# Optimization experiments

Hardware: AMD Instinct MI355X
Metric: run time of the kernel (lower is better)

The kernel has to match this reference:

```python
import jax, jax.numpy as jnp
import numpy as np

N, E, F_IN, F_OUT = 8192, 1024, 256, 256


def setup_inputs() -> dict:
    key = jax.random.key(0)
    k1, k2, k3, k4 = jax.random.split(key, 4)
    X = jax.random.normal(k1, (N, F_IN), dtype=jnp.float32)
    # binary incidence matrix: node i belongs to hyperedge j with p=0.05
    H = (jax.random.uniform(k2, (N, E)) < 0.05).astype(jnp.float32)
    W = jax.random.normal(k3, (F_OUT, F_IN), dtype=jnp.float32) * (1.0 / np.sqrt(F_IN))
    b = jax.random.normal(k4, (F_OUT,), dtype=jnp.float32) * 0.01
    return {"X": X, "H": H, "W": W, "b": b}


def reference(X, H, W, b):
    # Dv = diag(row sums of H), De = diag(col sums of H)
    dv = jnp.sum(H, axis=1)                      # [N] node degrees
    de = jnp.sum(H, axis=0)                      # [E] edge degrees
    dv_inv_sqrt = 1.0 / jnp.sqrt(dv)             # inv of sqrt(Dv) (diagonal)
    de_inv = 1.0 / de                            # inv of De (diagonal)
    # diagonal matrices realized as broadcast scalings (same math, no N x N).
    Xs = X * dv_inv_sqrt[:, None]
    M = H.T @ Xs                                 # H^T (...)          [E, F]
    M = M * de_inv[:, None]                      # De^-1 (...)        [E, F]
    X_new = (H @ M) * dv_inv_sqrt[:, None]       # Dv^-1/2 H (...)    [N, F]
    return X_new @ W.T + b                       # nn.Linear
```

## Files before the change

kernel.cpp:

```cpp
#include <hip/hip_runtime.h>
#include <hip/hip_bf16.h>
#include <stdint.h>

typedef __attribute__((ext_vector_type(8))) short bf16x8;
typedef __attribute__((ext_vector_type(4))) float f32x4;
typedef __attribute__((ext_vector_type(4))) unsigned int u32x4;
typedef __attribute__((ext_vector_type(2))) unsigned int u32x2;
typedef unsigned short u16;
typedef unsigned int u32;
typedef unsigned long long u64;

#define N_NODES 8192
#define N_EDGES 1024
#define F_DIM   256
#define EMAX 512
#define NMAX 128
#define NSEG 512
#define SEGR 16

__device__ __forceinline__ u16 f2bf(float f) {
    union { float f; u32 u; } v; v.f = f;
    u32 u = v.u;
    u = (u + 0x7FFFu + ((u >> 16) & 1u)) >> 16;
    return (u16)u;
}
__device__ __forceinline__ float bflo(u32 p) {
    union { u32 u; float f; } v; v.u = p << 16; return v.f;
}
__device__ __forceinline__ float bfhi(u32 p) {
    union { u32 u; float f; } v; v.u = p & 0xffff0000u; return v.f;
}

__global__ void prep_count(const float* __restrict__ H, const float* __restrict__ X,
                           float* __restrict__ dv, u16* __restrict__ nlist,
                           u16* __restrict__ Xs, u16* __restrict__ cnt_seg) {
    __shared__ u32 colp[4][64][4];
    const int tid = threadIdx.x;
    const int wv = tid >> 6;
    const int lane = tid & 63;
    const int n0 = blockIdx.x * SEGR + wv * 4;

    f32x4 hv[4][4];
    f32x4 xv[4];
#pragma unroll
    for (int r = 0; r < 4; ++r) {
        const int n = n0 + r;
#pragma unroll
        for (int q = 0; q < 4; ++q)
            hv[r][q] = *(const f32x4*)(&H[(size_t)n * N_EDGES + q * 256 + lane * 4]);
        xv[r] = *(const f32x4*)(&X[(size_t)n * F_DIM + lane * 4]);
    }

    u32 cpk[4] = {0u, 0u, 0u, 0u};
#pragma unroll
    for (int r = 0; r < 4; ++r) {
        const int n = n0 + r;
        u32 m16 = 0u;
#pragma unroll
        for (int q = 0; q < 4; ++q)
#pragma unroll
            for (int j = 0; j < 4; ++j) {
                const u32 nz = (hv[r][q][j] != 0.f) ? 1u : 0u;
                m16 |= nz << (q * 4 + j);
                cpk[q] += nz << (8 * j);
            }
        const u32 cl = (u32)__popc(m16);
        u32 x = cl;
#pragma unroll
        for (int d = 1; d < 64; d <<= 1) {
            const u32 t = __shfl_up(x, d, 64);
            if (lane >= d) x += t;
        }
        const u32 total = __shfl(x, 63, 64);
        u32 pos = x - cl;
        u16* nrow = &nlist[(size_t)n * NMAX];
        u32 m = m16;
        while (m) {
            const int bidx = __builtin_ctz(m);
            m &= m - 1;
            const int col = ((bidx >> 2) << 8) + lane * 4 + (bidx & 3);
            if (pos < NMAX) nrow[pos] = (u16)col;
            ++pos;
        }
        if (lane == 0) dv[n] = (float)total;
        const float s = rsqrtf((float)total);
        u32x2 pk;
        pk[0] = (u32)f2bf(xv[r][0] * s) | ((u32)f2bf(xv[r][1] * s) << 16);
        pk[1] = (u32)f2bf(xv[r][2] * s) | ((u32)f2bf(xv[r][3] * s) << 16);
        *(u32x2*)(&Xs[(size_t)n * F_DIM + lane * 4]) = pk;
    }
#pragma unroll
    for (int q = 0; q < 4; ++q) colp[wv][lane][q] = cpk[q];
    __syncthreads();
    const int q = tid >> 6, l = tid & 63;
    const u32 sum = colp[0][l][q] + colp[1][l][q] + colp[2][l][q] + colp[3][l][q];
    const int s = blockIdx.x;
#pragma unroll
    for (int j = 0; j < 4; ++j) {
        const int col = q * 256 + l * 4 + j;
        cnt_seg[(size_t)col * NSEG + s] = (u16)((sum >> (8 * j)) & 0xffu);
    }
}

__global__ void prefix_seg(const u16* __restrict__ cnt_seg, u16* __restrict__ base,
                           u32* __restrict__ cnt_e) {
    const int tid = threadIdx.x;
    const int wv = tid >> 6, lane = tid & 63;
    const int e = blockIdx.x * 4 + wv;
    union { u32x4 v; u16 c[8]; } in;
    in.v = *(const u32x4*)(&cnt_seg[(size_t)e * NSEG + lane * 8]);
    u32 run = 0, pre[8];
#pragma unroll
    for (int k = 0; k < 8; ++k) { pre[k] = run; run += in.c[k]; }
    u32 x = run;
#pragma unroll
    for (int d = 1; d < 64; d <<= 1) {
        const u32 t = __shfl_up(x, d, 64);
        if (lane >= d) x += t;
    }
    const u32 excl = x - run;
    union { u32x4 v; u16 o[8]; } out;
#pragma unroll
    for (int k = 0; k < 8; ++k) out.o[k] = (u16)(excl + pre[k]);
    *(u32x4*)(&base[(size_t)e * NSEG + lane * 8]) = out.v;
    if (lane == 63) cnt_e[e] = x;
}

__global__ void scatter_build(const float* __restrict__ H, const u16* __restrict__ base,
                              u16* __restrict__ elist) {
    const int t = threadIdx.x;
    const int s = blockIdx.x;
    const int c0 = t * 4;
    const int r0 = s * SEGR;
    f32x4 v[16];
#pragma unroll
    for (int rr = 0; rr < SEGR; ++rr)
        v[rr] = *(const f32x4*)(&H[(size_t)(r0 + rr) * N_EDGES + c0]);
    u32 b[4];
#pragma unroll
    for (int j = 0; j < 4; ++j) b[j] = base[(size_t)(c0 + j) * NSEG + s];
#pragma unroll
    for (int rr = 0; rr < SEGR; ++rr) {
        const int r = r0 + rr;
#pragma unroll
        for (int j = 0; j < 4; ++j)
            if (v[rr][j] != 0.f) {
                if (b[j] < EMAX) elist[(size_t)(c0 + j) * EMAX + b[j]] = (u16)r;
                b[j]++;
            }
    }
}

__global__ void spmm1(const u16* __restrict__ Xs, const u32* __restrict__ cnt_e,
                      const u16* __restrict__ elist, float* __restrict__ M) {
    __shared__ u16 lst[EMAX];
    __shared__ float red[16 * F_DIM];
    const int tid = threadIdx.x;
    const int wv = tid >> 6, lane = tid & 63;
    const int e = blockIdx.x;
    const int cnt = min((int)cnt_e[e], EMAX);
    if (tid < 256)
        ((u32*)lst)[tid] = ((const u32*)&elist[(size_t)e * EMAX])[tid];
    __syncthreads();

    const int half = lane >> 5;
    const int l32 = lane & 31;
    const int npairs = (cnt + 1) >> 1;
    const int len = (npairs + 7) >> 3;
    const int p0 = wv * len;
    const int p1 = min(p0 + len, npairs);
    float a[8] = {};
#pragma unroll 4
    for (int p = p0; p < p1; ++p) {
        const int idx = 2 * p + half;
        if (idx < cnt) {
            const int nn = lst[idx];
            const u32x4 pk = *(const u32x4*)(&Xs[(size_t)nn * F_DIM + l32 * 8]);
#pragma unroll
            for (int k = 0; k < 4; ++k) { a[2 * k] += bflo(pk[k]); a[2 * k + 1] += bfhi(pk[k]); }
        }
    }
    f32x4 r0 = {a[0], a[1], a[2], a[3]};
    f32x4 r1 = {a[4], a[5], a[6], a[7]};
    *(f32x4*)(&red[(wv * 2 + half) * F_DIM + l32 * 8]) = r0;
    *(f32x4*)(&red[(wv * 2 + half) * F_DIM + l32 * 8 + 4]) = r1;
    __syncthreads();
    if (tid < F_DIM) {
        float s = 0.f;
#pragma unroll
        for (int w = 0; w < 16; ++w) s += red[w * F_DIM + tid];
        M[(size_t)e * F_DIM + tid] = s;
    }
}

__global__ void gemm_we(const float* __restrict__ M, const u32* __restrict__ cnt_e,
                        const float* __restrict__ W, u16* __restrict__ M2) {
    __shared__ u16 As[64 * 72];
    __shared__ u16 Bs[64 * 72];
    const int tid = threadIdx.x;
    const int lane = tid & 63;
    const int wave = tid >> 6;
    const int wm = wave >> 1, wn = wave & 1;
    const int row16 = lane & 15;
    const int quad = lane >> 4;

    const int e0 = blockIdx.y * 64;
    const int j0 = blockIdx.x * 64;

    const int sr = tid >> 2;
    const int fb = (tid & 3) * 16;

    const float dei = 1.f / (float)cnt_e[e0 + sr];

    f32x4 acc[2][2] = {};

    for (int k = 0; k < 256; k += 64) {
#pragma unroll
        for (int s2 = 0; s2 < 4; ++s2) {
            f32x4 a = *(const f32x4*)(&M[(size_t)(e0 + sr) * F_DIM + k + fb + s2 * 4]);
            u32x2 pk;
            pk[0] = (u32)f2bf(a[0] * dei) | ((u32)f2bf(a[1] * dei) << 16);
            pk[1] = (u32)f2bf(a[2] * dei) | ((u32)f2bf(a[3] * dei) << 16);
            *(u32x2*)(&As[sr * 72 + fb + s2 * 4]) = pk;
            f32x4 w = *(const f32x4*)(&W[(size_t)(j0 + sr) * F_DIM + k + fb + s2 * 4]);
            pk[0] = (u32)f2bf(w[0]) | ((u32)f2bf(w[1]) << 16);
            pk[1] = (u32)f2bf(w[2]) | ((u32)f2bf(w[3]) << 16);
            *(u32x2*)(&Bs[sr * 72 + fb + s2 * 4]) = pk;
        }
        __syncthreads();
#pragma unroll
        for (int ks = 0; ks < 2; ++ks) {
            bf16x8 af[2], bfr[2];
#pragma unroll
            for (int t = 0; t < 2; ++t) {
                af[t]  = *(const bf16x8*)(&As[(wm * 32 + t * 16 + row16) * 72 + ks * 32 + quad * 8]);
                bfr[t] = *(const bf16x8*)(&Bs[(wn * 32 + t * 16 + row16) * 72 + ks * 32 + quad * 8]);
            }
#pragma unroll
            for (int tm = 0; tm < 2; tm++)
#pragma unroll
                for (int tn = 0; tn < 2; tn++)
                    acc[tm][tn] = __builtin_amdgcn_mfma_f32_16x16x32_bf16(
                        af[tm], bfr[tn], acc[tm][tn], 0, 0, 0);
        }
        __syncthreads();
    }

#pragma unroll
    for (int tm = 0; tm < 2; tm++) {
#pragma unroll
        for (int tn = 0; tn < 2; tn++) {
            const int col = j0 + wn * 32 + tn * 16 + row16;
#pragma unroll
            for (int r = 0; r < 4; r++) {
                const int row = e0 + wm * 32 + tm * 16 + quad * 4 + r;
                M2[(size_t)row * F_DIM + col] = f2bf(acc[tm][tn][r]);
            }
        }
    }
}

__global__ void spmm2(const u16* __restrict__ M2, const float* __restrict__ dv,
                      const u16* __restrict__ nlist, const float* __restrict__ bias,
                      float* __restrict__ out) {
    __shared__ u16 nl[4 * NMAX];
    __shared__ float red2[4][2][F_DIM];
    const int tid = threadIdx.x;
    const int wv = tid >> 6, lane = tid & 63;
    const int n = blockIdx.x * 4 + wv;
    if (tid < 256)
        ((u32*)nl)[tid] = ((const u32*)&nlist[(size_t)blockIdx.x * 4 * NMAX])[tid];
    __syncthreads();
    const float dvn = dv[n];
    const int cnt = min((int)dvn, NMAX);
    const u16* lst = &nl[wv * NMAX];
    const int half = lane >> 5;
    const int l32 = lane & 31;
    float a[8] = {};
    const int npairs = (cnt + 1) >> 1;
#pragma unroll 4
    for (int p = 0; p < npairs; ++p) {
        const int idx = 2 * p + half;
        if (idx < cnt) {
            const int e = lst[idx];
            const u32x4 pk = *(const u32x4*)(&M2[(size_t)e * F_DIM + l32 * 8]);
#pragma unroll
            for (int k = 0; k < 4; ++k) { a[2 * k] += bflo(pk[k]); a[2 * k + 1] += bfhi(pk[k]); }
        }
    }
    f32x4 r0 = {a[0], a[1], a[2], a[3]};
    f32x4 r1 = {a[4], a[5], a[6], a[7]};
    *(f32x4*)(&red2[wv][half][l32 * 8]) = r0;
    *(f32x4*)(&red2[wv][half][l32 * 8 + 4]) = r1;
    const float s = rsqrtf(dvn);
    const f32x4 bb = *(const f32x4*)(&bias[lane * 4]);
    f32x4 r;
#pragma unroll
    for (int k = 0; k < 4; ++k)
        r[k] = (red2[wv][0][lane * 4 + k] + red2[wv][1][lane * 4 + k]) * s + bb[k];
    *(f32x4*)(&out[(size_t)n * F_DIM + lane * 4]) = r;
}

extern "C" void kernel_launch(void* const* d_in, const int* in_sizes, int n_in,
                              void* d_out, int out_size, void* d_ws, size_t ws_size,
                              hipStream_t stream) {
    (void)in_sizes; (void)n_in; (void)out_size; (void)ws_size;
    const float* X = (const float*)d_in[0];
    const float* H = (const float*)d_in[1];
    const float* W = (const float*)d_in[2];
    const float* b = (const float*)d_in[3];
    float* out = (float*)d_out;

    char* ws = (char*)d_ws;
    float* dv      = (float*)(ws);
    u32*   cnt_e   = (u32*)(ws + 0x8000);
    u16*   cnt_seg = (u16*)(ws + 0x10000);
    u16*   base    = (u16*)(ws + 0x110000);
    u16*   nlist   = (u16*)(ws + 0x210000);
    u16*   elist   = (u16*)(ws + 0x410000);
    u16*   Xs      = (u16*)(ws + 0x510000);
    float* M       = (float*)(ws + 0x910000);
    u16*   M2      = (u16*)(ws + 0xA10000);

    prep_count<<<NSEG, 256, 0, stream>>>(H, X, dv, nlist, Xs, cnt_seg);
    prefix_seg<<<256, 256, 0, stream>>>(cnt_seg, base, cnt_e);
    scatter_build<<<NSEG, 256, 0, stream>>>(H, base, elist);
    spmm1<<<N_EDGES, 512, 0, stream>>>(Xs, cnt_e, elist, M);
    gemm_we<<<dim3(4, 16), 256, 0, stream>>>(M, cnt_e, W, M2);
    spmm2<<<N_NODES / 4, 256, 0, stream>>>(M2, dv, nlist, b, out);
}
```

Before: 140.4 us.

## Fuse all six stages into one cooperative persistent kernel with grid syncs

Replaces the six separate kernel launches with a single cooperative kernel of 256 blocks that runs each stage in turn, separated by grid.sync. The second pass over H in scatter_build is removed by caching per-row bitmasks in shared memory. The segment layout changes to 32 rows per block and the prefix scan is reorganised. The aim is to remove launch gaps and the redundant H reread. The cost is that the prefix and GEMM stages now use only 16 or 64 blocks while the rest of the grid waits, and every grid barrier adds overhead.

```diff
diff --git a/kernel.cpp b/kernel.cpp
--- a/kernel.cpp
+++ b/kernel.cpp
@@ -1,6 +1,9 @@
 #include <hip/hip_runtime.h>
+#include <hip/hip_cooperative_groups.h>
 #include <hip/hip_bf16.h>
 #include <stdint.h>
+
+namespace cg = cooperative_groups;
 
 typedef __attribute__((ext_vector_type(8))) short bf16x8;
 typedef __attribute__((ext_vector_type(4))) float f32x4;
@@ -15,8 +18,10 @@
 #define F_DIM   256
 #define EMAX 512
 #define NMAX 128
-#define NSEG 512
-#define SEGR 16
+#define NSEG 256
+#define SEGR 32
+#define NBLK 256
+#define NTHR 512
 
 __device__ __forceinline__ u16 f2bf(float f) {
     union { float f; u32 u; } v; v.f = f;
@@ -31,274 +36,286 @@
     union { u32 u; float f; } v; v.u = p & 0xffff0000u; return v.f;
 }
 
-__global__ void prep_count(const float* __restrict__ H, const float* __restrict__ X,
-                           float* __restrict__ dv, u16* __restrict__ nlist,
-                           u16* __restrict__ Xs, u16* __restrict__ cnt_seg) {
-    __shared__ u32 colp[4][64][4];
+struct SMem {
+    u16 hmask[SEGR][64];
+    union {
+        u32 colp[8][64][4];
+        u32 sums[64][8];
+        struct {
+            u32   lst[4][256];
+            float red[4][4][256];
+        } p4;
+        struct {
+            u16 As[64 * 72];
+            u16 Bs[64 * 72];
+        } p5;
+        struct {
+            u32   nl[2048];
+            float red2[8][2][256];
+        } p6;
+    } u;
+};
+
+__global__ void __launch_bounds__(NTHR) mega(
+    const float* __restrict__ H, const float* __restrict__ X,
+    const float* __restrict__ W, const float* __restrict__ bias,
+    float* __restrict__ out,
+    float* __restrict__ dv, u32* __restrict__ cnt_e,
+    u16* __restrict__ cnt_seg, u16* __restrict__ base,
+    u16* __restrict__ nlist, u16* __restrict__ elist,
+    u16* __restrict__ Xs, float* __restrict__ M, u16* __restrict__ M2)
+{
+    __shared__ SMem sm;
+    cg::grid_group grid = cg::this_grid();
     const int tid = threadIdx.x;
+    const int blk = blockIdx.x;
     const int wv = tid >> 6;
     const int lane = tid & 63;
-    const int n0 = blockIdx.x * SEGR + wv * 4;
-
-    f32x4 hv[4][4];
-    f32x4 xv[4];
-#pragma unroll
-    for (int r = 0; r < 4; ++r) {
-        const int n = n0 + r;
-#pragma unroll
-        for (int q = 0; q < 4; ++q)
-            hv[r][q] = *(const f32x4*)(&H[(size_t)n * N_EDGES + q * 256 + lane * 4]);
-        xv[r] = *(const f32x4*)(&X[(size_t)n * F_DIM + lane * 4]);
-    }
-
-    u32 cpk[4] = {0u, 0u, 0u, 0u};
-#pragma unroll
-    for (int r = 0; r < 4; ++r) {
-        const int n = n0 + r;
-        u32 m16 = 0u;
-#pragma unroll
-        for (int q = 0; q < 4; ++q)
-#pragma unroll
-            for (int j = 0; j < 4; ++j) {
-                const u32 nz = (hv[r][q][j] != 0.f) ? 1u : 0u;
-                m16 |= nz << (q * 4 + j);
-                cpk[q] += nz << (8 * j);
-            }
-        const u32 cl = (u32)__popc(m16);
-        u32 x = cl;
-#pragma unroll
-        for (int d = 1; d < 64; d <<= 1) {
-            const u32 t = __shfl_up(x, d, 64);
-            if (lane >= d) x += t;
-        }
-        const u32 total = __shfl(x, 63, 64);
-        u32 pos = x - cl;
-        u16* nrow = &nlist[(size_t)n * NMAX];
-        u32 m = m16;
-        while (m) {
-            const int bidx = __builtin_ctz(m);
-            m &= m - 1;
-            const int col = ((bidx >> 2) << 8) + lane * 4 + (bidx & 3);
-            if (pos < NMAX) nrow[pos] = (u16)col;
-            ++pos;
-        }
-        if (lane == 0) dv[n] = (float)total;
-        const float s = rsqrtf((float)total);
-        u32x2 pk;
-        pk[0] = (u32)f2bf(xv[r][0] * s) | ((u32)f2bf(xv[r][1] * s) << 16);
-        pk[1] = (u32)f2bf(xv[r][2] * s) | ((u32)f2bf(xv[r][3] * s) << 16);
-        *(u32x2*)(&Xs[(size_t)n * F_DIM + lane * 4]) = pk;
-    }
-#pragma unroll
-    for (int q = 0; q < 4; ++q) colp[wv][lane][q] = cpk[q];
-    __syncthreads();
-    const int q = tid >> 6, l = tid & 63;
-    const u32 sum = colp[0][l][q] + colp[1][l][q] + colp[2][l][q] + colp[3][l][q];
-    const int s = blockIdx.x;
-#pragma unroll
-    for (int j = 0; j < 4; ++j) {
-        const int col = q * 256 + l * 4 + j;
-        cnt_seg[(size_t)col * NSEG + s] = (u16)((sum >> (8 * j)) & 0xffu);
-    }
-}
-
-__global__ void prefix_seg(const u16* __restrict__ cnt_seg, u16* __restrict__ base,
-                           u32* __restrict__ cnt_e) {
-    const int tid = threadIdx.x;
-    const int wv = tid >> 6, lane = tid & 63;
-    const int e = blockIdx.x * 4 + wv;
-    union { u32x4 v; u16 c[8]; } in;
-    in.v = *(const u32x4*)(&cnt_seg[(size_t)e * NSEG + lane * 8]);
-    u32 run = 0, pre[8];
-#pragma unroll
-    for (int k = 0; k < 8; ++k) { pre[k] = run; run += in.c[k]; }
-    u32 x = run;
-#pragma unroll
-    for (int d = 1; d < 64; d <<= 1) {
-        const u32 t = __shfl_up(x, d, 64);
-        if (lane >= d) x += t;
-    }
-    const u32 excl = x - run;
-    union { u32x4 v; u16 o[8]; } out;
-#pragma unroll
-    for (int k = 0; k < 8; ++k) out.o[k] = (u16)(excl + pre[k]);
-    *(u32x4*)(&base[(size_t)e * NSEG + lane * 8]) = out.v;
-    if (lane == 63) cnt_e[e] = x;
-}
-
-__global__ void scatter_build(const float* __restrict__ H, const u16* __restrict__ base,
-                              u16* __restrict__ elist) {
-    const int t = threadIdx.x;
-    const int s = blockIdx.x;
-    const int c0 = t * 4;
-    const int r0 = s * SEGR;
-    f32x4 v[16];
-#pragma unroll
-    for (int rr = 0; rr < SEGR; ++rr)
-        v[rr] = *(const f32x4*)(&H[(size_t)(r0 + rr) * N_EDGES + c0]);
-    u32 b[4];
-#pragma unroll
-    for (int j = 0; j < 4; ++j) b[j] = base[(size_t)(c0 + j) * NSEG + s];
-#pragma unroll
-    for (int rr = 0; rr < SEGR; ++rr) {
-        const int r = r0 + rr;
-#pragma unroll
-        for (int j = 0; j < 4; ++j)
-            if (v[rr][j] != 0.f) {
-                if (b[j] < EMAX) elist[(size_t)(c0 + j) * EMAX + b[j]] = (u16)r;
-                b[j]++;
-            }
-    }
-}
-
-__global__ void spmm1(const u16* __restrict__ Xs, const u32* __restrict__ cnt_e,
-                      const u16* __restrict__ elist, float* __restrict__ M) {
-    __shared__ u16 lst[EMAX];
-    __shared__ float red[16 * F_DIM];
-    const int tid = threadIdx.x;
-    const int wv = tid >> 6, lane = tid & 63;
-    const int e = blockIdx.x;
-    const int cnt = min((int)cnt_e[e], EMAX);
-    if (tid < 256)
-        ((u32*)lst)[tid] = ((const u32*)&elist[(size_t)e * EMAX])[tid];
-    __syncthreads();
-
-    const int half = lane >> 5;
-    const int l32 = lane & 31;
-    const int npairs = (cnt + 1) >> 1;
-    const int len = (npairs + 7) >> 3;
-    const int p0 = wv * len;
-    const int p1 = min(p0 + len, npairs);
-    float a[8] = {};
-#pragma unroll 4
-    for (int p = p0; p < p1; ++p) {
-        const int idx = 2 * p + half;
-        if (idx < cnt) {
-            const int nn = lst[idx];
-            const u32x4 pk = *(const u32x4*)(&Xs[(size_t)nn * F_DIM + l32 * 8]);
-#pragma unroll
-            for (int k = 0; k < 4; ++k) { a[2 * k] += bflo(pk[k]); a[2 * k + 1] += bfhi(pk[k]); }
-        }
-    }
-    f32x4 r0 = {a[0], a[1], a[2], a[3]};
-    f32x4 r1 = {a[4], a[5], a[6], a[7]};
-    *(f32x4*)(&red[(wv * 2 + half) * F_DIM + l32 * 8]) = r0;
-    *(f32x4*)(&red[(wv * 2 + half) * F_DIM + l32 * 8 + 4]) = r1;
-    __syncthreads();
-    if (tid < F_DIM) {
-        float s = 0.f;
-#pragma unroll
-        for (int w = 0; w < 16; ++w) s += red[w * F_DIM + tid];
-        M[(size_t)e * F_DIM + tid] = s;
-    }
-}
-
-__global__ void gemm_we(const float* __restrict__ M, const u32* __restrict__ cnt_e,
-                        const float* __restrict__ W, u16* __restrict__ M2) {
-    __shared__ u16 As[64 * 72];
-    __shared__ u16 Bs[64 * 72];
-    const int tid = threadIdx.x;
-    const int lane = tid & 63;
-    const int wave = tid >> 6;
-    const int wm = wave >> 1, wn = wave & 1;
-    const int row16 = lane & 15;
-    const int quad = lane >> 4;
-
-    const int e0 = blockIdx.y * 64;
-    const int j0 = blockIdx.x * 64;
-
-    const int sr = tid >> 2;
-    const int fb = (tid & 3) * 16;
-
-    const float dei = 1.f / (float)cnt_e[e0 + sr];
-
-    f32x4 acc[2][2] = {};
-
-    for (int k = 0; k < 256; k += 64) {
-#pragma unroll
-        for (int s2 = 0; s2 < 4; ++s2) {
-            f32x4 a = *(const f32x4*)(&M[(size_t)(e0 + sr) * F_DIM + k + fb + s2 * 4]);
+
+    {
+        const int n0 = blk * SEGR + wv * 4;
+        f32x4 hv[4][4], xv[4];
+#pragma unroll
+        for (int r = 0; r < 4; ++r) {
+            const int n = n0 + r;
+#pragma unroll
+            for (int q = 0; q < 4; ++q)
+                hv[r][q] = *(const f32x4*)(&H[(size_t)n * N_EDGES + q * 256 + lane * 4]);
+            xv[r] = *(const f32x4*)(&X[(size_t)n * F_DIM + lane * 4]);
+        }
+        u32 cpk[4] = {0u, 0u, 0u, 0u};
+#pragma unroll
+        for (int r = 0; r < 4; ++r) {
+            const int n = n0 + r;
+            u32 m16 = 0u;
+#pragma unroll
+            for (int q = 0; q < 4; ++q)
+#pragma unroll
+                for (int j = 0; j < 4; ++j) {
+                    const u32 nz = (hv[r][q][j] != 0.f) ? 1u : 0u;
+                    m16 |= nz << (q * 4 + j);
+                    cpk[q] += nz << (8 * j);
+                }
+            sm.hmask[wv * 4 + r][lane] = (u16)m16;
+            const u32 cl = (u32)__popc(m16);
+            u32 x = cl;
+#pragma unroll
+            for (int d = 1; d < 64; d <<= 1) {
+                const u32 t = __shfl_up(x, d, 64);
+                if (lane >= d) x += t;
+            }
+            const u32 total = __shfl(x, 63, 64);
+            u32 pos = x - cl;
+            u16* nrow = &nlist[(size_t)n * NMAX];
+            u32 m = m16;
+            while (m) {
+                const int bidx = __builtin_ctz(m);
+                m &= m - 1;
+                const int col = ((bidx >> 2) << 8) + lane * 4 + (bidx & 3);
+                if (pos < NMAX) nrow[pos] = (u16)col;
+                ++pos;
+            }
+            if (lane == 0) dv[n] = (float)total;
+            const float s = rsqrtf((float)total);
             u32x2 pk;
-            pk[0] = (u32)f2bf(a[0] * dei) | ((u32)f2bf(a[1] * dei) << 16);
-            pk[1] = (u32)f2bf(a[2] * dei) | ((u32)f2bf(a[3] * dei) << 16);
-            *(u32x2*)(&As[sr * 72 + fb + s2 * 4]) = pk;
-            f32x4 w = *(const f32x4*)(&W[(size_t)(j0 + sr) * F_DIM + k + fb + s2 * 4]);
-            pk[0] = (u32)f2bf(w[0]) | ((u32)f2bf(w[1]) << 16);
-            pk[1] = (u32)f2bf(w[2]) | ((u32)f2bf(w[3]) << 16);
-            *(u32x2*)(&Bs[sr * 72 + fb + s2 * 4]) = pk;
-        }
-        __syncthreads();
-#pragma unroll
-        for (int ks = 0; ks < 2; ++ks) {
-            bf16x8 af[2], bfr[2];
-#pragma unroll
-            for (int t = 0; t < 2; ++t) {
-                af[t]  = *(const bf16x8*)(&As[(wm * 32 + t * 16 + row16) * 72 + ks * 32 + quad * 8]);
-                bfr[t] = *(const bf16x8*)(&Bs[(wn * 32 + t * 16 + row16) * 72 + ks * 32 + quad * 8]);
-            }
-#pragma unroll
-            for (int tm = 0; tm < 2; tm++)
-#pragma unroll
-                for (int tn = 0; tn < 2; tn++)
-                    acc[tm][tn] = __builtin_amdgcn_mfma_f32_16x16x32_bf16(
-                        af[tm], bfr[tn], acc[tm][tn], 0, 0, 0);
-        }
-        __syncthreads();
-    }
-
-#pragma unroll
-    for (int tm = 0; tm < 2; tm++) {
-#pragma unroll
-        for (int tn = 0; tn < 2; tn++) {
-            const int col = j0 + wn * 32 + tn * 16 + row16;
-#pragma unroll
-            for (int r = 0; r < 4; r++) {
-                const int row = e0 + wm * 32 + tm * 16 + quad * 4 + r;
-                M2[(size_t)row * F_DIM + col] = f2bf(acc[tm][tn][r]);
-            }
-        }
-    }
-}
-
-__global__ void spmm2(const u16* __restrict__ M2, const float* __restrict__ dv,
-                      const u16* __restrict__ nlist, const float* __restrict__ bias,
-                      float* __restrict__ out) {
-    __shared__ u16 nl[4 * NMAX];
-    __shared__ float red2[4][2][F_DIM];
-    const int tid = threadIdx.x;
-    const int wv = tid >> 6, lane = tid & 63;
-    const int n = blockIdx.x * 4 + wv;
-    if (tid < 256)
-        ((u32*)nl)[tid] = ((const u32*)&nlist[(size_t)blockIdx.x * 4 * NMAX])[tid];
-    __syncthreads();
-    const float dvn = dv[n];
-    const int cnt = min((int)dvn, NMAX);
-    const u16* lst = &nl[wv * NMAX];
-    const int half = lane >> 5;
-    const int l32 = lane & 31;
-    float a[8] = {};
-    const int npairs = (cnt + 1) >> 1;
-#pragma unroll 4
-    for (int p = 0; p < npairs; ++p) {
-        const int idx = 2 * p + half;
-        if (idx < cnt) {
-            const int e = lst[idx];
-            const u32x4 pk = *(const u32x4*)(&M2[(size_t)e * F_DIM + l32 * 8]);
-#pragma unroll
-            for (int k = 0; k < 4; ++k) { a[2 * k] += bflo(pk[k]); a[2 * k + 1] += bfhi(pk[k]); }
-        }
-    }
-    f32x4 r0 = {a[0], a[1], a[2], a[3]};
-    f32x4 r1 = {a[4], a[5], a[6], a[7]};
-    *(f32x4*)(&red2[wv][half][l32 * 8]) = r0;
-    *(f32x4*)(&red2[wv][half][l32 * 8 + 4]) = r1;
-    const float s = rsqrtf(dvn);
-    const f32x4 bb = *(const f32x4*)(&bias[lane * 4]);
-    f32x4 r;
-#pragma unroll
-    for (int k = 0; k < 4; ++k)
-        r[k] = (red2[wv][0][lane * 4 + k] + red2[wv][1][lane * 4 + k]) * s + bb[k];
-    *(f32x4*)(&out[(size_t)n * F_DIM + lane * 4]) = r;
+            pk[0] = (u32)f2bf(xv[r][0] * s) | ((u32)f2bf(xv[r][1] * s) << 16);
+            pk[1] = (u32)f2bf(xv[r][2] * s) | ((u32)f2bf(xv[r][3] * s) << 16);
+            *(u32x2*)(&Xs[(size_t)n * F_DIM + lane * 4]) = pk;
+        }
+#pragma unroll
+        for (int q = 0; q < 4; ++q) sm.u.colp[wv][lane][q] = cpk[q];
+        __syncthreads();
+        if (tid < 256) {
+            const int q = tid >> 6, l = tid & 63;
+            u32 sum = 0;
+#pragma unroll
+            for (int w = 0; w < 8; ++w) sum += sm.u.colp[w][l][q];
+            u32x2 st;
+            st[0] = (sum & 0xffu) | (((sum >> 8) & 0xffu) << 16);
+            st[1] = ((sum >> 16) & 0xffu) | (((sum >> 24) & 0xffu) << 16);
+            *(u32x2*)(&cnt_seg[(size_t)blk * N_EDGES + q * 256 + l * 4]) = st;
+        }
+    }
+    __threadfence();
+    grid.sync();
+
+    if (blk < 16) {
+        const int el = tid & 63;
+        const int ch = tid >> 6;
+        const int e = blk * 64 + el;
+        u32 s1 = 0;
+#pragma unroll 8
+        for (int k = 0; k < 32; ++k)
+            s1 += cnt_seg[(size_t)(ch * 32 + k) * N_EDGES + e];
+        sm.u.sums[el][ch] = s1;
+        __syncthreads();
+        u32 run = 0;
+        for (int cc = 0; cc < ch; ++cc) run += sm.u.sums[el][cc];
+#pragma unroll 8
+        for (int k = 0; k < 32; ++k) {
+            const size_t idx = (size_t)(ch * 32 + k) * N_EDGES + e;
+            const u32 cv = cnt_seg[idx];
+            base[idx] = (u16)run;
+            run += cv;
+        }
+        if (ch == 7) cnt_e[e] = run;
+    }
+    __threadfence();
+    grid.sync();
+
+    {
+        const int c0 = tid * 2;
+        const u32 bb = *(const u32*)(&base[(size_t)blk * N_EDGES + c0]);
+        u32 b0 = bb & 0xffffu, b1 = bb >> 16;
+        const int q = c0 >> 8;
+        const int widx = (c0 & 255) >> 2;
+        const int bit0 = q * 4 + (c0 & 3);
+        const int r0g = blk * SEGR;
+        u16* el0 = &elist[(size_t)c0 * EMAX];
+        u16* el1 = &elist[(size_t)(c0 + 1) * EMAX];
+#pragma unroll 8
+        for (int r = 0; r < SEGR; ++r) {
+            const u32 mrow = sm.hmask[r][widx];
+            if ((mrow >> bit0) & 1u) { if (b0 < EMAX) el0[b0] = (u16)(r0g + r); b0++; }
+            if ((mrow >> (bit0 + 1)) & 1u) { if (b1 < EMAX) el1[b1] = (u16)(r0g + r); b1++; }
+        }
+    }
+    __threadfence();
+    grid.sync();
+
+    {
+        const int g = wv >> 1;
+        const int w2 = wv & 1;
+        const int e = blk * 4 + g;
+        const int tg = w2 * 64 + lane;
+        sm.u.p4.lst[g][tg]       = ((const u32*)&elist[(size_t)e * EMAX])[tg];
+        sm.u.p4.lst[g][tg + 128] = ((const u32*)&elist[(size_t)e * EMAX])[tg + 128];
+        const int cnt = min((int)cnt_e[e], EMAX);
+        __syncthreads();
+        const int half = lane >> 5, l32 = lane & 31;
+        const int npairs = (cnt + 1) >> 1;
+        const int len = (npairs + 1) >> 1;
+        const int p0 = w2 * len, p1 = min(p0 + len, npairs);
+        const u16* lst16 = (const u16*)sm.u.p4.lst[g];
+        float a[8] = {};
+#pragma unroll 8
+        for (int p = p0; p < p1; ++p) {
+            const int idx = 2 * p + half;
+            if (idx < cnt) {
+                const int nn = lst16[idx];
+                const u32x4 pk = *(const u32x4*)(&Xs[(size_t)nn * F_DIM + l32 * 8]);
+#pragma unroll
+                for (int k = 0; k < 4; ++k) { a[2*k] += bflo(pk[k]); a[2*k+1] += bfhi(pk[k]); }
+            }
+        }
+        f32x4 r0 = {a[0], a[1], a[2], a[3]};
+        f32x4 r1 = {a[4], a[5], a[6], a[7]};
+        *(f32x4*)(&sm.u.p4.red[g][w2 * 2 + half][l32 * 8]) = r0;
+        *(f32x4*)(&sm.u.p4.red[g][w2 * 2 + half][l32 * 8 + 4]) = r1;
+        __syncthreads();
+        const int g2 = tid >> 7, f = tid & 127;
+        float s0 = 0.f, s1 = 0.f;
+#pragma unroll
+        for (int w = 0; w < 4; ++w) {
+            s0 += sm.u.p4.red[g2][w][f];
+            s1 += sm.u.p4.red[g2][w][f + 128];
+        }
+        M[(size_t)(blk * 4 + g2) * F_DIM + f] = s0;
+        M[(size_t)(blk * 4 + g2) * F_DIM + f + 128] = s1;
+    }
+    __threadfence();
+    grid.sync();
+
+    if (blk < 64) {
+        const int e0 = (blk >> 2) * 64;
+        const int j0 = (blk & 3) * 64;
+        const int row16 = lane & 15, quad = lane >> 4;
+        const int wm = wv >> 2, wn = wv & 3;
+        const int sr = tid >> 3;
+        const int fb = (tid & 7) * 8;
+        const float dei = 1.f / (float)cnt_e[e0 + sr];
+        f32x4 acc[2] = {};
+        for (int k = 0; k < 256; k += 64) {
+            __syncthreads();
+            f32x4 m0 = *(const f32x4*)(&M[(size_t)(e0 + sr) * F_DIM + k + fb]);
+            f32x4 m1 = *(const f32x4*)(&M[(size_t)(e0 + sr) * F_DIM + k + fb + 4]);
+            u32x2 pk;
+            pk[0] = (u32)f2bf(m0[0] * dei) | ((u32)f2bf(m0[1] * dei) << 16);
+            pk[1] = (u32)f2bf(m0[2] * dei) | ((u32)f2bf(m0[3] * dei) << 16);
+            *(u32x2*)(&sm.u.p5.As[sr * 72 + fb]) = pk;
+            pk[0] = (u32)f2bf(m1[0] * dei) | ((u32)f2bf(m1[1] * dei) << 16);
+            pk[1] = (u32)f2bf(m1[2] * dei) | ((u32)f2bf(m1[3] * dei) << 16);
+            *(u32x2*)(&sm.u.p5.As[sr * 72 + fb + 4]) = pk;
+            f32x4 w0 = *(const f32x4*)(&W[(size_t)(j0 + sr) * F_DIM + k + fb]);
+            f32x4 w1 = *(const f32x4*)(&W[(size_t)(j0 + sr) * F_DIM + k + fb + 4]);
+            pk[0] = (u32)f2bf(w0[0]) | ((u32)f2bf(w0[1]) << 16);
+            pk[1] = (u32)f2bf(w0[2]) | ((u32)f2bf(w0[3]) << 16);
+            *(u32x2*)(&sm.u.p5.Bs[sr * 72 + fb]) = pk;
+            pk[0] = (u32)f2bf(w1[0]) | ((u32)f2bf(w1[1]) << 16);
+            pk[1] = (u32)f2bf(w1[2]) | ((u32)f2bf(w1[3]) << 16);
+            *(u32x2*)(&sm.u.p5.Bs[sr * 72 + fb + 4]) = pk;
+            __syncthreads();
+#pragma unroll
+            for (int ks = 0; ks < 2; ++ks) {
+                bf16x8 af[2], bf;
+#pragma unroll
+                for (int t = 0; t < 2; ++t)
+                    af[t] = *(const bf16x8*)(&sm.u.p5.As[(wm * 32 + t * 16 + row16) * 72 + ks * 32 + quad * 8]);
+                bf = *(const bf16x8*)(&sm.u.p5.Bs[(wn * 16 + row16) * 72 + ks * 32 + quad * 8]);
+#pragma unroll
+                for (int t = 0; t < 2; ++t)
+                    acc[t] = __builtin_amdgcn_mfma_f32_16x16x32_bf16(af[t], bf, acc[t], 0, 0, 0);
+            }
+        }
+#pragma unroll
+        for (int t = 0; t < 2; ++t)
+#pragma unroll
+            for (int r = 0; r < 4; ++r)
+                M2[(size_t)(e0 + wm * 32 + t * 16 + quad * 4 + r) * F_DIM + j0 + wn * 16 + row16] =
+                    f2bf(acc[t][r]);
+    }
+    __threadfence();
+    grid.sync();
+
+    {
+        const u32* gn = (const u32*)&nlist[(size_t)blk * 32 * NMAX];
+#pragma unroll
+        for (int k = 0; k < 4; ++k) sm.u.p6.nl[tid + k * 512] = gn[tid + k * 512];
+        __syncthreads();
+        const int half = lane >> 5, l32 = lane & 31;
+        const f32x4 bb4 = *(const f32x4*)(&bias[lane * 4]);
+#pragma unroll
+        for (int rnd = 0; rnd < 4; ++rnd) {
+            const int nloc = rnd * 8 + wv;
+            const int n = blk * 32 + nloc;
+            const float dvn = dv[n];
+            const int cnt = min((int)dvn, NMAX);
+            const u16* lst = (const u16*)&sm.u.p6.nl[nloc * 64];
+            float a[8] = {};
+            const int npairs = (cnt + 1) >> 1;
+#pragma unroll 8
+            for (int p = 0; p < npairs; ++p) {
+                const int idx = 2 * p + half;
+                if (idx < cnt) {
+                    const int e = lst[idx];
+                    const u32x4 pk = *(const u32x4*)(&M2[(size_t)e * F_DIM + l32 * 8]);
+#pragma unroll
+                    for (int k = 0; k < 4; ++k) { a[2*k] += bflo(pk[k]); a[2*k+1] += bfhi(pk[k]); }
+                }
+            }
+            f32x4 r0 = {a[0], a[1], a[2], a[3]};
+            f32x4 r1 = {a[4], a[5], a[6], a[7]};
+            *(f32x4*)(&sm.u.p6.red2[wv][half][l32 * 8]) = r0;
+            *(f32x4*)(&sm.u.p6.red2[wv][half][l32 * 8 + 4]) = r1;
+            const float s = rsqrtf(dvn);
+            f32x4 r;
+#pragma unroll
+            for (int k = 0; k < 4; ++k)
+                r[k] = (sm.u.p6.red2[wv][0][lane * 4 + k] +
+                        sm.u.p6.red2[wv][1][lane * 4 + k]) * s + bb4[k];
+            *(f32x4*)(&out[(size_t)n * F_DIM + lane * 4]) = r;
+        }
+    }
 }
 
 extern "C" void kernel_launch(void* const* d_in, const int* in_sizes, int n_in,
@@ -315,17 +332,17 @@
     float* dv      = (float*)(ws);
     u32*   cnt_e   = (u32*)(ws + 0x8000);
     u16*   cnt_seg = (u16*)(ws + 0x10000);
-    u16*   base    = (u16*)(ws + 0x110000);
-    u16*   nlist   = (u16*)(ws + 0x210000);
-    u16*   elist   = (u16*)(ws + 0x410000);
-    u16*   Xs      = (u16*)(ws + 0x510000);
-    float* M       = (float*)(ws + 0x910000);
-    u16*   M2      = (u16*)(ws + 0xA10000);
-
-    prep_count<<<NSEG, 256, 0, stream>>>(H, X, dv, nlist, Xs, cnt_seg);
-    prefix_seg<<<256, 256, 0, stream>>>(cnt_seg, base, cnt_e);
-    scatter_build<<<NSEG, 256, 0, stream>>>(H, base, elist);
-    spmm1<<<N_EDGES, 512, 0, stream>>>(Xs, cnt_e, elist, M);
-    gemm_we<<<dim3(4, 16), 256, 0, stream>>>(M, cnt_e, W, M2);
-    spmm2<<<N_NODES / 4, 256, 0, stream>>>(M2, dv, nlist, b, out);
-}
+    u16*   base    = (u16*)(ws + 0x90000);
+    u16*   nlist   = (u16*)(ws + 0x110000);
+    u16*   elist   = (u16*)(ws + 0x310000);
+    u16*   Xs      = (u16*)(ws + 0x410000);
+    float* M       = (float*)(ws + 0x810000);
+    u16*   M2      = (u16*)(ws + 0x910000);
+
+    void* args[14] = {
+        (void*)&H, (void*)&X, (void*)&W, (void*)&b, (void*)&out,
+        (void*)&dv, (void*)&cnt_e, (void*)&cnt_seg, (void*)&base,
+        (void*)&nlist, (void*)&elist, (void*)&Xs, (void*)&M, (void*)&M2
+    };
+    hipLaunchCooperativeKernel((void*)mega, dim3(NBLK), dim3(NTHR), args, 0, stream);
+}
```

Measured after the change: 515.6 us. +267.2%, slower.

## Replace per-edge CSR build with transposed bitmask incidence consumed directly in spmm1

Applied to the files above, without the earlier changes.

The prep kernel now packs H into a transposed bitmask (32 nodes per u32 word per edge) instead of computing segment counts, prefix sums and a scattered edge list. This removes the prefix_seg and scatter_build kernels and a second full read of H. spmm1 walks the bitmask words with ctz, derives the edge degree from popcounts, applies De^-1 itself and writes bf16, so gemm_we loads bf16 directly. The cost is bit-scan overhead and uneven per-wave work in spmm1, plus a bit-transposition in shared memory in prep.

```diff
diff --git a/kernel.cpp b/kernel.cpp
--- a/kernel.cpp
+++ b/kernel.cpp
@@ -13,10 +13,8 @@
 #define N_NODES 8192
 #define N_EDGES 1024
 #define F_DIM   256
-#define EMAX 512
 #define NMAX 128
-#define NSEG 512
-#define SEGR 16
+#define NSEG 256
 
 __device__ __forceinline__ u16 f2bf(float f) {
     union { float f; u32 u; } v; v.f = f;
@@ -31,17 +29,18 @@
     union { u32 u; float f; } v; v.u = p & 0xffff0000u; return v.f;
 }
 
-__global__ void prep_count(const float* __restrict__ H, const float* __restrict__ X,
-                           float* __restrict__ dv, u16* __restrict__ nlist,
-                           u16* __restrict__ Xs, u16* __restrict__ cnt_seg) {
-    __shared__ u32 colp[4][64][4];
+__global__ __launch_bounds__(512) void prep(
+    const float* __restrict__ H, const float* __restrict__ X,
+    float* __restrict__ dv, u16* __restrict__ nlist,
+    u16* __restrict__ Xs, u32* __restrict__ HbT) {
+    __shared__ u16 hmask[32][64];
     const int tid = threadIdx.x;
     const int wv = tid >> 6;
     const int lane = tid & 63;
-    const int n0 = blockIdx.x * SEGR + wv * 4;
-
-    f32x4 hv[4][4];
-    f32x4 xv[4];
+    const int blk = blockIdx.x;
+    const int n0 = blk * 32 + wv * 4;
+
+    f32x4 hv[4][4], xv[4];
 #pragma unroll
     for (int r = 0; r < 4; ++r) {
         const int n = n0 + r;
@@ -51,7 +50,6 @@
         xv[r] = *(const f32x4*)(&X[(size_t)n * F_DIM + lane * 4]);
     }
 
-    u32 cpk[4] = {0u, 0u, 0u, 0u};
 #pragma unroll
     for (int r = 0; r < 4; ++r) {
         const int n = n0 + r;
@@ -59,11 +57,9 @@
 #pragma unroll
         for (int q = 0; q < 4; ++q)
 #pragma unroll
-            for (int j = 0; j < 4; ++j) {
-                const u32 nz = (hv[r][q][j] != 0.f) ? 1u : 0u;
-                m16 |= nz << (q * 4 + j);
-                cpk[q] += nz << (8 * j);
-            }
+            for (int j = 0; j < 4; ++j)
+                m16 |= ((hv[r][q][j] != 0.f) ? 1u : 0u) << (q * 4 + j);
+        hmask[wv * 4 + r][lane] = (u16)m16;
         const u32 cl = (u32)__popc(m16);
         u32 x = cl;
 #pragma unroll
@@ -89,112 +85,78 @@
         pk[1] = (u32)f2bf(xv[r][2] * s) | ((u32)f2bf(xv[r][3] * s) << 16);
         *(u32x2*)(&Xs[(size_t)n * F_DIM + lane * 4]) = pk;
     }
-#pragma unroll
-    for (int q = 0; q < 4; ++q) colp[wv][lane][q] = cpk[q];
-    __syncthreads();
-    const int q = tid >> 6, l = tid & 63;
-    const u32 sum = colp[0][l][q] + colp[1][l][q] + colp[2][l][q] + colp[3][l][q];
-    const int s = blockIdx.x;
-#pragma unroll
-    for (int j = 0; j < 4; ++j) {
-        const int col = q * 256 + l * 4 + j;
-        cnt_seg[(size_t)col * NSEG + s] = (u16)((sum >> (8 * j)) & 0xffu);
-    }
-}
-
-__global__ void prefix_seg(const u16* __restrict__ cnt_seg, u16* __restrict__ base,
-                           u32* __restrict__ cnt_e) {
-    const int tid = threadIdx.x;
-    const int wv = tid >> 6, lane = tid & 63;
-    const int e = blockIdx.x * 4 + wv;
-    union { u32x4 v; u16 c[8]; } in;
-    in.v = *(const u32x4*)(&cnt_seg[(size_t)e * NSEG + lane * 8]);
-    u32 run = 0, pre[8];
-#pragma unroll
-    for (int k = 0; k < 8; ++k) { pre[k] = run; run += in.c[k]; }
-    u32 x = run;
-#pragma unroll
-    for (int d = 1; d < 64; d <<= 1) {
-        const u32 t = __shfl_up(x, d, 64);
-        if (lane >= d) x += t;
-    }
-    const u32 excl = x - run;
-    union { u32x4 v; u16 o[8]; } out;
-#pragma unroll
-    for (int k = 0; k < 8; ++k) out.o[k] = (u16)(excl + pre[k]);
-    *(u32x4*)(&base[(size_t)e * NSEG + lane * 8]) = out.v;
-    if (lane == 63) cnt_e[e] = x;
-}
-
-__global__ void scatter_build(const float* __restrict__ H, const u16* __restrict__ base,
-                              u16* __restrict__ elist) {
-    const int t = threadIdx.x;
-    const int s = blockIdx.x;
-    const int c0 = t * 4;
-    const int r0 = s * SEGR;
-    f32x4 v[16];
-#pragma unroll
-    for (int rr = 0; rr < SEGR; ++rr)
-        v[rr] = *(const f32x4*)(&H[(size_t)(r0 + rr) * N_EDGES + c0]);
-    u32 b[4];
-#pragma unroll
-    for (int j = 0; j < 4; ++j) b[j] = base[(size_t)(c0 + j) * NSEG + s];
-#pragma unroll
-    for (int rr = 0; rr < SEGR; ++rr) {
-        const int r = r0 + rr;
-#pragma unroll
-        for (int j = 0; j < 4; ++j)
-            if (v[rr][j] != 0.f) {
-                if (b[j] < EMAX) elist[(size_t)(c0 + j) * EMAX + b[j]] = (u16)r;
-                b[j]++;
+    __syncthreads();
+#pragma unroll
+    for (int eo = 0; eo < 2; ++eo) {
+        const int e = tid + eo * 512;
+        const int widx = (e & 255) >> 2;
+        const int bit = ((e >> 8) << 2) + (e & 3);
+        u32 w = 0u;
+#pragma unroll
+        for (int r = 0; r < 32; ++r)
+            w |= (u32)((hmask[r][widx] >> bit) & 1u) << r;
+        HbT[(size_t)e * NSEG + blk] = w;
+    }
+}
+
+__global__ __launch_bounds__(512) void spmm1(
+    const u16* __restrict__ Xs, const u32* __restrict__ HbT,
+    u16* __restrict__ Mb) {
+    __shared__ u32 words[NSEG];
+    __shared__ float red[16][2][128];
+    __shared__ u32 wcnt[8];
+    const int tid = threadIdx.x;
+    const int wv = tid >> 6;
+    const int lane = tid & 63;
+    const int e = blockIdx.x;
+    if (tid < NSEG) words[tid] = HbT[(size_t)e * NSEG + tid];
+    __syncthreads();
+    const int half = lane >> 5, l32 = lane & 31;
+    float a[8] = {};
+    u32 cnt = 0;
+    for (int s = wv * 32; s < wv * 32 + 32; ++s) {
+        u32 w = words[s];
+        cnt += (u32)__popc(w);
+        const int nb = s * 32;
+        while (w) {
+            const int b0 = __builtin_ctz(w); w &= w - 1;
+            const int b1 = w ? __builtin_ctz(w) : -1;
+            if (w) w &= w - 1;
+            const int b = half ? b1 : b0;
+            if (b >= 0) {
+                const int n = nb + b;
+                const u32x4 pk = *(const u32x4*)(&Xs[(size_t)n * F_DIM + l32 * 8]);
+                a[0] += bflo(pk[0]); a[1] += bfhi(pk[0]);
+                a[2] += bflo(pk[1]); a[3] += bfhi(pk[1]);
+                a[4] += bflo(pk[2]); a[5] += bfhi(pk[2]);
+                a[6] += bflo(pk[3]); a[7] += bfhi(pk[3]);
             }
-    }
-}
-
-__global__ void spmm1(const u16* __restrict__ Xs, const u32* __restrict__ cnt_e,
-                      const u16* __restrict__ elist, float* __restrict__ M) {
-    __shared__ u16 lst[EMAX];
-    __shared__ float red[16 * F_DIM];
-    const int tid = threadIdx.x;
-    const int wv = tid >> 6, lane = tid & 63;
-    const int e = blockIdx.x;
-    const int cnt = min((int)cnt_e[e], EMAX);
-    if (tid < 256)
-        ((u32*)lst)[tid] = ((const u32*)&elist[(size_t)e * EMAX])[tid];
-    __syncthreads();
-
-    const int half = lane >> 5;
-    const int l32 = lane & 31;
-    const int npairs = (cnt + 1) >> 1;
-    const int len = (npairs + 7) >> 3;
-    const int p0 = wv * len;
-    const int p1 = min(p0 + len, npairs);
-    float a[8] = {};
-#pragma unroll 4
-    for (int p = p0; p < p1; ++p) {
-        const int idx = 2 * p + half;
-        if (idx < cnt) {
-            const int nn = lst[idx];
-            const u32x4 pk = *(const u32x4*)(&Xs[(size_t)nn * F_DIM + l32 * 8]);
-#pragma unroll
-            for (int k = 0; k < 4; ++k) { a[2 * k] += bflo(pk[k]); a[2 * k + 1] += bfhi(pk[k]); }
-        }
-    }
+        }
+    }
+    const int ws = wv * 2 + half;
     f32x4 r0 = {a[0], a[1], a[2], a[3]};
     f32x4 r1 = {a[4], a[5], a[6], a[7]};
-    *(f32x4*)(&red[(wv * 2 + half) * F_DIM + l32 * 8]) = r0;
-    *(f32x4*)(&red[(wv * 2 + half) * F_DIM + l32 * 8 + 4]) = r1;
+    *(f32x4*)(&red[ws][0][l32 * 4]) = r0;
+    *(f32x4*)(&red[ws][1][l32 * 4]) = r1;
+    if (lane == 0) wcnt[wv] = cnt;
     __syncthreads();
     if (tid < F_DIM) {
+        const int f = tid;
+        const int pl = (f >> 2) & 1;
+        const int ix = ((f >> 3) << 2) | (f & 3);
         float s = 0.f;
 #pragma unroll
-        for (int w = 0; w < 16; ++w) s += red[w * F_DIM + tid];
-        M[(size_t)e * F_DIM + tid] = s;
-    }
-}
-
-__global__ void gemm_we(const float* __restrict__ M, const u32* __restrict__ cnt_e,
-                        const float* __restrict__ W, u16* __restrict__ M2) {
+        for (int w = 0; w < 16; ++w) s += red[w][pl][ix];
+        u32 de = 0;
+#pragma unroll
+        for (int w = 0; w < 8; ++w) de += wcnt[w];
+        Mb[(size_t)e * F_DIM + f] = f2bf(s / (float)de);
+    }
+}
+
+__global__ __launch_bounds__(256) void gemm_we(
+    const u16* __restrict__ Mb, const float* __restrict__ W,
+    u16* __restrict__ M2) {
     __shared__ u16 As[64 * 72];
     __shared__ u16 Bs[64 * 72];
     const int tid = threadIdx.x;
@@ -210,19 +172,17 @@
     const int sr = tid >> 2;
     const int fb = (tid & 3) * 16;
 
-    const float dei = 1.f / (float)cnt_e[e0 + sr];
-
     f32x4 acc[2][2] = {};
 
     for (int k = 0; k < 256; k += 64) {
+        const u32x4 a0 = *(const u32x4*)(&Mb[(size_t)(e0 + sr) * F_DIM + k + fb]);
+        const u32x4 a1 = *(const u32x4*)(&Mb[(size_t)(e0 + sr) * F_DIM + k + fb + 8]);
+        *(u32x4*)(&As[sr * 72 + fb]) = a0;
+        *(u32x4*)(&As[sr * 72 + fb + 8]) = a1;
 #pragma unroll
         for (int s2 = 0; s2 < 4; ++s2) {
-            f32x4 a = *(const f32x4*)(&M[(size_t)(e0 + sr) * F_DIM + k + fb + s2 * 4]);
+            f32x4 w = *(const f32x4*)(&W[(size_t)(j0 + sr) * F_DIM + k + fb + s2 * 4]);
             u32x2 pk;
-            pk[0] = (u32)f2bf(a[0] * dei) | ((u32)f2bf(a[1] * dei) << 16);
-            pk[1] = (u32)f2bf(a[2] * dei) | ((u32)f2bf(a[3] * dei) << 16);
-            *(u32x2*)(&As[sr * 72 + fb + s2 * 4]) = pk;
-            f32x4 w = *(const f32x4*)(&W[(size_t)(j0 + sr) * F_DIM + k + fb + s2 * 4]);
             pk[0] = (u32)f2bf(w[0]) | ((u32)f2bf(w[1]) << 16);
             pk[1] = (u32)f2bf(w[2]) | ((u32)f2bf(w[3]) << 16);
             *(u32x2*)(&Bs[sr * 72 + fb + s2 * 4]) = pk;
@@ -260,11 +220,12 @@
     }
 }
 
-__global__ void spmm2(const u16* __restrict__ M2, const float* __restrict__ dv,
-                      const u16* __restrict__ nlist, const float* __restrict__ bias,
-                      float* __restrict__ out) {
+__global__ __launch_bounds__(256) void spmm2(
+    const u16* __restrict__ M2, const float* __restrict__ dv,
+    const u16* __restrict__ nlist, const float* __restrict__ bias,
+    float* __restrict__ out) {
     __shared__ u16 nl[4 * NMAX];
-    __shared__ float red2[4][2][F_DIM];
+    __shared__ float red2[4][2][2][128];
     const int tid = threadIdx.x;
     const int wv = tid >> 6, lane = tid & 63;
     const int n = blockIdx.x * 4 + wv;
@@ -284,20 +245,23 @@
         if (idx < cnt) {
             const int e = lst[idx];
             const u32x4 pk = *(const u32x4*)(&M2[(size_t)e * F_DIM + l32 * 8]);
-#pragma unroll
-            for (int k = 0; k < 4; ++k) { a[2 * k] += bflo(pk[k]); a[2 * k + 1] += bfhi(pk[k]); }
+            a[0] += bflo(pk[0]); a[1] += bfhi(pk[0]);
+            a[2] += bflo(pk[1]); a[3] += bfhi(pk[1]);
+            a[4] += bflo(pk[2]); a[5] += bfhi(pk[2]);
+            a[6] += bflo(pk[3]); a[7] += bfhi(pk[3]);
         }
     }
     f32x4 r0 = {a[0], a[1], a[2], a[3]};
     f32x4 r1 = {a[4], a[5], a[6], a[7]};
-    *(f32x4*)(&red2[wv][half][l32 * 8]) = r0;
-    *(f32x4*)(&red2[wv][half][l32 * 8 + 4]) = r1;
+    *(f32x4*)(&red2[wv][half][0][l32 * 4]) = r0;
+    *(f32x4*)(&red2[wv][half][1][l32 * 4]) = r1;
     const float s = rsqrtf(dvn);
     const f32x4 bb = *(const f32x4*)(&bias[lane * 4]);
+    const f32x4 v0 = *(const f32x4*)(&red2[wv][0][lane & 1][(lane >> 1) * 4]);
+    const f32x4 v1 = *(const f32x4*)(&red2[wv][1][lane & 1][(lane >> 1) * 4]);
     f32x4 r;
 #pragma unroll
-    for (int k = 0; k < 4; ++k)
-        r[k] = (red2[wv][0][lane * 4 + k] + red2[wv][1][lane * 4 + k]) * s + bb[k];
+    for (int k = 0; k < 4; ++k) r[k] = (v0[k] + v1[k]) * s + bb[k];
     *(f32x4*)(&out[(size_t)n * F_DIM + lane * 4]) = r;
 }
 
@@ -312,20 +276,15 @@
     float* out = (float*)d_out;
 
     char* ws = (char*)d_ws;
-    float* dv      = (float*)(ws);
-    u32*   cnt_e   = (u32*)(ws + 0x8000);
-    u16*   cnt_seg = (u16*)(ws + 0x10000);
-    u16*   base    = (u16*)(ws + 0x110000);
-    u16*   nlist   = (u16*)(ws + 0x210000);
-    u16*   elist   = (u16*)(ws + 0x410000);
-    u16*   Xs      = (u16*)(ws + 0x510000);
-    float* M       = (float*)(ws + 0x910000);
-    u16*   M2      = (u16*)(ws + 0xA10000);
-
-    prep_count<<<NSEG, 256, 0, stream>>>(H, X, dv, nlist, Xs, cnt_seg);
-    prefix_seg<<<256, 256, 0, stream>>>(cnt_seg, base, cnt_e);
-    scatter_build<<<NSEG, 256, 0, stream>>>(H, base, elist);
-    spmm1<<<N_EDGES, 512, 0, stream>>>(Xs, cnt_e, elist, M);
-    gemm_we<<<dim3(4, 16), 256, 0, stream>>>(M, cnt_e, W, M2);
+    float* dv    = (float*)(ws);
+    u32*   HbT   = (u32*)(ws + 0x10000);
+    u16*   nlist = (u16*)(ws + 0x110000);
+    u16*   Xs    = (u16*)(ws + 0x310000);
+    u16*   Mb    = (u16*)(ws + 0x710000);
+    u16*   M2    = (u16*)(ws + 0x790000);
+
+    prep<<<NSEG, 512, 0, stream>>>(H, X, dv, nlist, Xs, HbT);
+    spmm1<<<N_EDGES, 512, 0, stream>>>(Xs, HbT, Mb);
+    gemm_we<<<dim3(4, 16), 256, 0, stream>>>(Mb, W, M2);
     spmm2<<<N_NODES / 4, 256, 0, stream>>>(M2, dv, nlist, b, out);
 }
```

New measurement: 132.3 us. 1.06x faster.
